# Optimization experiments

Measured on AMD Instinct MI355X. Metric: run time of the kernel, lower is better.

The kernel has to match this reference:

```python
import jax, jax.numpy as jnp
import numpy as np

B, M, T, F_IN, H = 16, 512, 64, 128, 128


def _gru_layer(x, wih, whh, bih, bhh):
    # x: [B, T, H_in]; torch nn.GRU gate math, single layer, h0 = 0
    Hh = whh.shape[1]

    def step(h_prev, x_t):
        gi = x_t @ wih.T + bih          # [B, 3H]
        gh = h_prev @ whh.T + bhh       # [B, 3H]
        i_r, i_z, i_n = jnp.split(gi, 3, axis=-1)
        h_r, h_z, h_n = jnp.split(gh, 3, axis=-1)
        r = jax.nn.sigmoid(i_r + h_r)
        z = jax.nn.sigmoid(i_z + h_z)
        n = jnp.tanh(i_n + r * h_n)
        h_new = (1.0 - z) * n + z * h_prev
        return h_new, h_new

    h0 = jnp.zeros((x.shape[0], Hh), x.dtype)
    _, ys = jax.lax.scan(step, h0, jnp.swapaxes(x, 0, 1))  # [T, B, H]
    return jnp.swapaxes(ys, 0, 1)                          # [B, T, H]


def setup_inputs() -> dict:
    key = jax.random.key(0)
    ks = jax.random.split(key, 12)
    s = 0.05

    def w(k, shape):
        return jax.random.normal(k, shape, jnp.float32) * s

    return {
        "X": jax.random.normal(ks[0], (B, M, T, F_IN), jnp.float32),
        "C": jax.random.normal(ks[1], (B, M, T), jnp.float32),
        "h_target": jax.random.normal(ks[2], (B, T, H), jnp.float32),
        "distance": jax.random.uniform(ks[3], (M,), jnp.float32),
        "lin_w": w(ks[4], (H, F_IN)), "lin_b": jnp.zeros((H,), jnp.float32),
        "mlp_w1": w(ks[5], (H, 2 * H)), "mlp_b1": jnp.zeros((H,), jnp.float32),
        "mlp_w2": w(ks[6], (1, H)), "mlp_b2": jnp.zeros((1,), jnp.float32),
        "lin2_w": w(ks[7], (1, 3)), "lin2_b": jnp.zeros((1,), jnp.float32),
        "gru_wih0": w(ks[8], (3 * H, H)), "gru_whh0": w(ks[9], (3 * H, H)),
        "gru_bih0": jnp.zeros((3 * H,), jnp.float32), "gru_bhh0": jnp.zeros((3 * H,), jnp.float32),
        "gru_wih1": w(ks[10], (3 * H, H)), "gru_whh1": w(ks[11], (3 * H, H)),
        "gru_bih1": jnp.zeros((3 * H,), jnp.float32), "gru_bhh1": jnp.zeros((3 * H,), jnp.float32),
    }


def reference(X, C, h_target, distance,
              lin_w, lin_b, mlp_w1, mlp_b1, mlp_w2, mlp_b2,
              lin2_w, lin2_b,
              gru_wih0, gru_whh0, gru_bih0, gru_bhh0,
              gru_wih1, gru_whh1, gru_bih1, gru_bhh1):
    # h: [B, M, T, H]
    h = jnp.einsum('bmtf,hf->bmth', X, lin_w) + lin_b
    # broadcast h_target over message dim M: [B, 1, T, H] -> [B, M, T, H]
    ht = jnp.broadcast_to(h_target[:, None, :, :], h.shape)
    cat = jnp.concatenate([ht, h], axis=-1)                    # [B, M, T, 2H]
    mlp_h = jax.nn.relu(jnp.einsum('bmtf,hf->bmth', cat, mlp_w1) + mlp_b1)
    w_msg = jnp.einsum('bmth,oh->bmto', mlp_h, mlp_w2) + mlp_b2  # [B, M, T, 1]
    # distance broadcast: [1, M, 1, 1] -> [B, M, T, 1]
    dist = jnp.broadcast_to(distance[None, :, None, None], w_msg.shape)
    coef = jnp.concatenate([C[..., None], dist, w_msg], axis=-1)  # [B, M, T, 3]
    learned_w = coef @ lin2_w.T + lin2_b                          # [B, M, T, 1]
    h_agg = jnp.sum(h * learned_w, axis=1)                        # [B, T, H]
    # 2-layer GRU (eval mode: no dropout)
    out0 = _gru_layer(h_agg, gru_wih0, gru_whh0, gru_bih0, gru_bhh0)
    out1 = _gru_layer(out0, gru_wih1, gru_whh1, gru_bih1, gru_bhh1)
    return out1
```

## Files before the change

### kernel.cpp

```cpp
#include <hip/hip_runtime.h>
#include <math.h>

#define NB 16
#define NM 512
#define NT 64
#define NF 128
#define NH 128
#define PADB 136

typedef short short8 __attribute__((ext_vector_type(8)));
typedef float floatx4 __attribute__((ext_vector_type(4)));

static __device__ __forceinline__ unsigned short f2b(float f) {
  union { float f; unsigned u; } v; v.f = f;
  unsigned r = v.u + 0x7fff + ((v.u >> 16) & 1);
  return (unsigned short)(r >> 16);
}
static __device__ __forceinline__ float b2f_us(unsigned short h) {
  union { unsigned u; float f; } v; v.u = ((unsigned)h) << 16; return v.f;
}

__global__ __launch_bounds__(128) void prep_kernel(
    const float* __restrict__ lin_w, const float* __restrict__ mlp_w1,
    const float* __restrict__ lin_b, const float* __restrict__ mlp_b1,
    unsigned short* __restrict__ WxBf, float* __restrict__ linT,
    float* __restrict__ ubase)
{
  const int tid = threadIdx.x;
  if (blockIdx.x < 128) {
    const int i = blockIdx.x;
    __shared__ float sw[128];
    __shared__ float rb[128];
    sw[tid] = mlp_w1[i * 256 + 128 + tid];
    __syncthreads();
    float s = 0.f;
#pragma unroll 16
    for (int k = 0; k < 128; k++) s += sw[k] * lin_w[k * 128 + tid];
    WxBf[i * 128 + tid] = f2b(s);
    rb[tid] = sw[tid] * lin_b[tid];
    __syncthreads();
    if (tid == 0) {
      float s2 = 0.f;
      for (int k = 0; k < 128; k++) s2 += rb[k];
      ubase[i] = mlp_b1[i] + s2;
    }
  } else {
    const int f = blockIdx.x - 128;
    linT[f * 128 + tid] = lin_w[tid * 128 + f];
  }
}

static __device__ __forceinline__ void tpose_tile(
    const float* __restrict__ in, float* __restrict__ outT,
    int R, int C, int S, int tileIdx)
{
  __shared__ float tile[32][33];
  const int tilesC = C >> 5;
  const int tr = tileIdx / tilesC, tc = tileIdx % tilesC;
  const int x = threadIdx.x & 31, y = threadIdx.x >> 5;
#pragma unroll
  for (int yy = y; yy < 32; yy += 8)
    tile[yy][x] = in[(size_t)(tr * 32 + yy) * S + tc * 32 + x];
  __syncthreads();
#pragma unroll
  for (int yy = y; yy < 32; yy += 8)
    outT[(size_t)(tc * 32 + yy) * R + tr * 32 + x] = tile[x][yy];
}

__global__ __launch_bounds__(256) void tpose_kernel(
    const float* __restrict__ wih0, const float* __restrict__ whh0,
    const float* __restrict__ wih1, const float* __restrict__ whh1,
    const float* __restrict__ mlp_w1,
    float* __restrict__ wih0T, float* __restrict__ whh0T,
    float* __restrict__ wih1T, float* __restrict__ whh1T,
    float* __restrict__ W1aT)
{
  const int b = blockIdx.x;
  if (b < 48)        tpose_tile(wih0,   wih0T, 384, 128, 128, b);
  else if (b < 96)   tpose_tile(whh0,   whh0T, 384, 128, 128, b - 48);
  else if (b < 144)  tpose_tile(wih1,   wih1T, 384, 128, 128, b - 96);
  else if (b < 192)  tpose_tile(whh1,   whh1T, 384, 128, 128, b - 144);
  else               tpose_tile(mlp_w1, W1aT,  128, 128, 256, b - 192);
}

__global__ __launch_bounds__(128) void u_kernel(
    const float* __restrict__ h_target, const float* __restrict__ W1aT,
    const float* __restrict__ ubase, float* __restrict__ u_out)
{
  const int bt = blockIdx.x, i = threadIdx.x;
  __shared__ float sht[128];
  sht[i] = h_target[bt * 128 + i];
  __syncthreads();
  float u = ubase[i];
#pragma unroll 16
  for (int k = 0; k < 128; k++) u += W1aT[k * 128 + i] * sht[k];
  u_out[bt * 128 + i] = u;
}

__global__ __launch_bounds__(256, 2) void pass1_kernel(
    const float* __restrict__ X, const float* __restrict__ C,
    const float* __restrict__ dist,
    const unsigned short* __restrict__ WxBf, const float* __restrict__ u_g,
    const float* __restrict__ mlp_w2, const float* __restrict__ mlp_b2,
    const float* __restrict__ lin2_w, const float* __restrict__ lin2_b,
    float* __restrict__ part, float* __restrict__ partls)
{
  const int blk = blockIdx.x;
  const int g = blk & 7, bt = blk >> 3;
  const int b = bt >> 6, t = bt & 63;
  const int tid = threadIdx.x;

  __shared__ unsigned short xb[64 * PADB];
  __shared__ unsigned short wxb[128 * PADB];
  __shared__ float u_sh[128], w2_sh[128], lw_sh[64];
  __shared__ float red[2][128];
  __shared__ float red_ls;

  const float* Xbase = X + (((size_t)(b * NM + g * 64)) * NT + t) * NF;
#pragma unroll
  for (int p = 0; p < 8; p++) {
    int idx = p * 256 + tid;
    int row = idx >> 5, c4 = idx & 31;
    float4 xv = *(const float4*)(Xbase + (size_t)row * NT * NF + c4 * 4);
    ushort4 h;
    h.x = f2b(xv.x); h.y = f2b(xv.y); h.z = f2b(xv.z); h.w = f2b(xv.w);
    *(ushort4*)&xb[row * PADB + c4 * 4] = h;
  }
  const unsigned* wsrc = (const unsigned*)WxBf;
  unsigned* wdst = (unsigned*)wxb;
#pragma unroll
  for (int p = 0; p < 32; p++) {
    int idx = p * 256 + tid;
    int row = idx >> 6, cu = idx & 63;
    wdst[row * (PADB / 2) + cu] = wsrc[idx];
  }
  if (tid < 128) { u_sh[tid] = u_g[bt * 128 + tid]; w2_sh[tid] = mlp_w2[tid]; }
  __syncthreads();

  const int w = tid >> 6, lane = tid & 63;
  const int col = lane & 15, quad = lane >> 4;
  short8 afr[4];
#pragma unroll
  for (int kc = 0; kc < 4; kc++)
    afr[kc] = *(const short8*)&xb[(w * 16 + col) * PADB + kc * 32 + quad * 8];
  floatx4 acc[8];
#pragma unroll
  for (int it = 0; it < 8; it++) acc[it] = {0.f, 0.f, 0.f, 0.f};
#pragma unroll
  for (int it = 0; it < 8; it++) {
#pragma unroll
    for (int kc = 0; kc < 4; kc++) {
      short8 bfr = *(const short8*)&wxb[(it * 16 + col) * PADB + kc * 32 + quad * 8];
      acc[it] = __builtin_amdgcn_mfma_f32_16x16x32_bf16(afr[kc], bfr, acc[it], 0, 0, 0);
    }
  }

  float w2l[8], ul[8];
#pragma unroll
  for (int it = 0; it < 8; it++) { w2l[it] = w2_sh[it * 16 + col]; ul[it] = u_sh[it * 16 + col]; }
  float vsum[4];
#pragma unroll
  for (int r = 0; r < 4; r++) {
    float v = 0.f;
#pragma unroll
    for (int it = 0; it < 8; it++) {
      float s = acc[it][r] + ul[it];
      v += w2l[it] * fmaxf(s, 0.f);
    }
    v += __shfl_xor(v, 1, 64);
    v += __shfl_xor(v, 2, 64);
    v += __shfl_xor(v, 4, 64);
    v += __shfl_xor(v, 8, 64);
    vsum[r] = v;
  }
  if (col == 0) {
    const float c0 = lin2_w[0], c1 = lin2_w[1], c2 = lin2_w[2];
    const float lb2 = lin2_b[0], mb2 = mlp_b2[0];
#pragma unroll
    for (int r = 0; r < 4; r++) {
      int ml = w * 16 + quad * 4 + r;
      int m = g * 64 + ml;
      float wmsg = vsum[r] + mb2;
      lw_sh[ml] = C[((size_t)b * NM + m) * NT + t] * c0 + dist[m] * c1 + wmsg * c2 + lb2;
    }
  }
  __syncthreads();

  const int f = tid & 127, half = tid >> 7;
  float xa = 0.f;
#pragma unroll 8
  for (int mm = half * 32; mm < half * 32 + 32; mm++)
    xa += lw_sh[mm] * b2f_us(xb[mm * PADB + f]);
  red[half][f] = xa;
  if (tid < 64) {
    float v = lw_sh[tid];
    v += __shfl_xor(v, 1, 64);
    v += __shfl_xor(v, 2, 64);
    v += __shfl_xor(v, 4, 64);
    v += __shfl_xor(v, 8, 64);
    v += __shfl_xor(v, 16, 64);
    v += __shfl_xor(v, 32, 64);
    if (tid == 0) red_ls = v;
  }
  __syncthreads();
  if (tid < 128) part[(size_t)blk * 128 + tid] = red[0][tid] + red[1][tid];
  if (tid == 128) partls[blk] = red_ls;
}

__global__ __launch_bounds__(384) void reduce_kernel(
    const float* __restrict__ part, const float* __restrict__ partls,
    const float* __restrict__ linT, const float* __restrict__ lin_b,
    const float* __restrict__ wih0T, const float* __restrict__ bih0,
    float* __restrict__ gi0)
{
  const int bt = blockIdx.x, j = threadIdx.x;
  __shared__ float sxa[128], shh[128];
  __shared__ float sls;
  if (j < 128) {
    float s = 0.f;
#pragma unroll
    for (int g2 = 0; g2 < 8; g2++) s += part[((size_t)bt * 8 + g2) * 128 + j];
    sxa[j] = s;
  }
  if (j == 128) {
    float s = 0.f;
#pragma unroll
    for (int g2 = 0; g2 < 8; g2++) s += partls[bt * 8 + g2];
    sls = s;
  }
  __syncthreads();
  if (j < 128) {
    float hv = sls * lin_b[j];
#pragma unroll 8
    for (int f2 = 0; f2 < 128; f2++) hv += linT[f2 * 128 + j] * sxa[f2];
    shh[j] = hv;
  }
  __syncthreads();
  float gacc = bih0[j];
#pragma unroll 16
  for (int k = 0; k < 128; k++) gacc += wih0T[k * 384 + j] * shh[k];
  gi0[(size_t)bt * 384 + j] = gacc;
}

__global__ __launch_bounds__(384, 2) void gi_kernel(
    const float* __restrict__ xin, const float* __restrict__ wihT,
    const float* __restrict__ bih, float* __restrict__ gi)
{
  __shared__ __align__(16) float xr[128];
  const int bt = blockIdx.x, j = threadIdx.x;
  if (j < 128) xr[j] = xin[bt * 128 + j];
  __syncthreads();
  float a0 = 0.f, a1 = 0.f, a2 = 0.f, a3 = 0.f;
#pragma unroll 8
  for (int k = 0; k < 128; k += 4) {
    a0 += wihT[(k    ) * 384 + j] * xr[k];
    a1 += wihT[(k + 1) * 384 + j] * xr[k + 1];
    a2 += wihT[(k + 2) * 384 + j] * xr[k + 2];
    a3 += wihT[(k + 3) * 384 + j] * xr[k + 3];
  }
  gi[(size_t)bt * 384 + j] = (a0 + a1) + (a2 + a3) + bih[j];
}

__global__ __launch_bounds__(384, 1) void gru_layer_kernel(
    const float* __restrict__ gi, const float* __restrict__ whhT,
    const float* __restrict__ bhh, float* __restrict__ out)
{
  const int b = blockIdx.x, j = threadIdx.x;
  __shared__ float sgi[64 * 384];
  __shared__ float hs[128], ghs[384];

  const float4* gsrc = (const float4*)(gi + (size_t)b * 64 * 384);
  float4* gdst = (float4*)sgi;
#pragma unroll
  for (int p = 0; p < 16; p++) gdst[p * 384 + j] = gsrc[p * 384 + j];

  float wreg[128];
#pragma unroll
  for (int k = 0; k < 128; k++) wreg[k] = whhT[k * 384 + j];
  const float bh = bhh[j];
  if (j < 128) hs[j] = 0.f;
  __syncthreads();

  for (int t = 0; t < NT; t++) {
    float a0 = 0.f, a1 = 0.f, a2 = 0.f, a3 = 0.f;
    const float4* h4 = (const float4*)hs;
#pragma unroll
    for (int k = 0; k < 32; k++) {
      float4 hv = h4[k];
      a0 += wreg[4 * k]     * hv.x;
      a1 += wreg[4 * k + 1] * hv.y;
      a2 += wreg[4 * k + 2] * hv.z;
      a3 += wreg[4 * k + 3] * hv.w;
    }
    ghs[j] = (a0 + a1) + (a2 + a3) + bh;
    __syncthreads();
    if (j < 128) {
      const float* gt = &sgi[t * 384];
      const float hprev = hs[j];
      const float r = 1.f / (1.f + __expf(-(gt[j] + ghs[j])));
      const float z = 1.f / (1.f + __expf(-(gt[128 + j] + ghs[128 + j])));
      float nx = gt[256 + j] + r * ghs[256 + j];
      nx = fmaxf(fminf(nx, 15.f), -15.f);
      const float e2 = __expf(2.f * nx);
      const float n = (e2 - 1.f) / (e2 + 1.f);
      const float hnew = (1.f - z) * n + z * hprev;
      hs[j] = hnew;
      out[((size_t)b * NT + t) * 128 + j] = hnew;
    }
    __syncthreads();
  }
}

extern "C" void kernel_launch(void* const* d_in, const int* in_sizes, int n_in,
                              void* d_out, int out_size, void* d_ws, size_t ws_size,
                              hipStream_t stream)
{
  const float* X        = (const float*)d_in[0];
  const float* C        = (const float*)d_in[1];
  const float* h_target = (const float*)d_in[2];
  const float* distance = (const float*)d_in[3];
  const float* lin_w    = (const float*)d_in[4];
  const float* lin_b    = (const float*)d_in[5];
  const float* mlp_w1   = (const float*)d_in[6];
  const float* mlp_b1   = (const float*)d_in[7];
  const float* mlp_w2   = (const float*)d_in[8];
  const float* mlp_b2   = (const float*)d_in[9];
  const float* lin2_w   = (const float*)d_in[10];
  const float* lin2_b   = (const float*)d_in[11];
  const float* wih0     = (const float*)d_in[12];
  const float* whh0     = (const float*)d_in[13];
  const float* bih0     = (const float*)d_in[14];
  const float* bhh0     = (const float*)d_in[15];
  const float* wih1     = (const float*)d_in[16];
  const float* whh1     = (const float*)d_in[17];
  const float* bih1     = (const float*)d_in[18];
  const float* bhh1     = (const float*)d_in[19];
  float* out = (float*)d_out;

  float* ws = (float*)d_ws;
  unsigned short* WxBf = (unsigned short*)ws;
  float* linT   = ws + 8192;
  float* u_buf  = ws + 24576;
  float* part   = ws + 155648;
  float* partls = ws + 1204224;
  float* gi     = ws + 1212416;
  float* out0   = ws + 1605632;
  float* W1aT   = ws + 1736704;
  float* wih0T  = ws + 1753088;
  float* whh0T  = ws + 1802240;
  float* wih1T  = ws + 1851392;
  float* whh1T  = ws + 1900544;
  float* ubase  = ws + 1949696;

  prep_kernel<<<256, 128, 0, stream>>>(lin_w, mlp_w1, lin_b, mlp_b1, WxBf, linT, ubase);
  tpose_kernel<<<208, 256, 0, stream>>>(wih0, whh0, wih1, whh1, mlp_w1,
      wih0T, whh0T, wih1T, whh1T, W1aT);
  u_kernel<<<NB * NT, 128, 0, stream>>>(h_target, W1aT, ubase, u_buf);
  pass1_kernel<<<NB * NT * 8, 256, 0, stream>>>(X, C, distance, WxBf, u_buf,
      mlp_w2, mlp_b2, lin2_w, lin2_b, part, partls);
  reduce_kernel<<<NB * NT, 384, 0, stream>>>(part, partls, linT, lin_b, wih0T, bih0, gi);
  gru_layer_kernel<<<NB, 384, 0, stream>>>(gi, whh0T, bhh0, out0);
  gi_kernel<<<NB * NT, 384, 0, stream>>>(out0, wih1T, bih1, gi);
  gru_layer_kernel<<<NB, 384, 0, stream>>>(gi, whh1T, bhh1, out);
}
```

Before: 605.8 us.

## Pre-swizzle weight fragments in global memory and keep X tile in fp32 LDS

The fused weight matrix is written by the prep kernel directly in MFMA B-fragment order, so pass1 reads B fragments straight from global/L2 instead of staging the whole weight matrix into LDS each block. X is kept in fp32 in LDS and converted to bf16 when the A fragments are built, so the aggregation step now uses fp32 X instead of the bf16-rounded values. With less LDS per block, the occupancy hint is raised from 2 to 4 blocks. The GRU gate math switches from fast __expf with manual tanh to expf/tanhf, which is more accurate but likely slower in the serial recurrence.

```diff
diff --git a/kernel.cpp b/kernel.cpp
--- a/kernel.cpp
+++ b/kernel.cpp
@@ -6,7 +6,7 @@
 #define NT 64
 #define NF 128
 #define NH 128
-#define PADB 136
+#define PAD4 132
 
 typedef short short8 __attribute__((ext_vector_type(8)));
 typedef float floatx4 __attribute__((ext_vector_type(4)));
@@ -16,14 +16,11 @@
   unsigned r = v.u + 0x7fff + ((v.u >> 16) & 1);
   return (unsigned short)(r >> 16);
 }
-static __device__ __forceinline__ float b2f_us(unsigned short h) {
-  union { unsigned u; float f; } v; v.u = ((unsigned)h) << 16; return v.f;
-}
 
 __global__ __launch_bounds__(128) void prep_kernel(
     const float* __restrict__ lin_w, const float* __restrict__ mlp_w1,
     const float* __restrict__ lin_b, const float* __restrict__ mlp_b1,
-    unsigned short* __restrict__ WxBf, float* __restrict__ linT,
+    unsigned short* __restrict__ WxFrag, float* __restrict__ linT,
     float* __restrict__ ubase)
 {
   const int tid = threadIdx.x;
@@ -36,7 +33,12 @@
     float s = 0.f;
 #pragma unroll 16
     for (int k = 0; k < 128; k++) s += sw[k] * lin_w[k * 128 + tid];
-    WxBf[i * 128 + tid] = f2b(s);
+    {
+      const int it = i >> 4, col = i & 15;
+      const int f = tid;
+      const int kc = f >> 5, quad = (f >> 3) & 3, jj = f & 7;
+      WxFrag[((it * 4 + kc) * 64 + quad * 16 + col) * 8 + jj] = f2b(s);
+    }
     rb[tid] = sw[tid] * lin_b[tid];
     __syncthreads();
     if (tid == 0) {
@@ -97,10 +99,10 @@
   u_out[bt * 128 + i] = u;
 }
 
-__global__ __launch_bounds__(256, 2) void pass1_kernel(
+__global__ __launch_bounds__(256, 4) void pass1_kernel(
     const float* __restrict__ X, const float* __restrict__ C,
     const float* __restrict__ dist,
-    const unsigned short* __restrict__ WxBf, const float* __restrict__ u_g,
+    const unsigned short* __restrict__ WxFrag, const float* __restrict__ u_g,
     const float* __restrict__ mlp_w2, const float* __restrict__ mlp_b2,
     const float* __restrict__ lin2_w, const float* __restrict__ lin2_b,
     float* __restrict__ part, float* __restrict__ partls)
@@ -110,8 +112,7 @@
   const int b = bt >> 6, t = bt & 63;
   const int tid = threadIdx.x;
 
-  __shared__ unsigned short xb[64 * PADB];
-  __shared__ unsigned short wxb[128 * PADB];
+  __shared__ float xs[64 * PAD4];
   __shared__ float u_sh[128], w2_sh[128], lw_sh[64];
   __shared__ float red[2][128];
   __shared__ float red_ls;
@@ -122,17 +123,7 @@
     int idx = p * 256 + tid;
     int row = idx >> 5, c4 = idx & 31;
     float4 xv = *(const float4*)(Xbase + (size_t)row * NT * NF + c4 * 4);
-    ushort4 h;
-    h.x = f2b(xv.x); h.y = f2b(xv.y); h.z = f2b(xv.z); h.w = f2b(xv.w);
-    *(ushort4*)&xb[row * PADB + c4 * 4] = h;
-  }
-  const unsigned* wsrc = (const unsigned*)WxBf;
-  unsigned* wdst = (unsigned*)wxb;
-#pragma unroll
-  for (int p = 0; p < 32; p++) {
-    int idx = p * 256 + tid;
-    int row = idx >> 6, cu = idx & 63;
-    wdst[row * (PADB / 2) + cu] = wsrc[idx];
+    *(float4*)&xs[row * PAD4 + c4 * 4] = xv;
   }
   if (tid < 128) { u_sh[tid] = u_g[bt * 128 + tid]; w2_sh[tid] = mlp_w2[tid]; }
   __syncthreads();
@@ -141,8 +132,13 @@
   const int col = lane & 15, quad = lane >> 4;
   short8 afr[4];
 #pragma unroll
-  for (int kc = 0; kc < 4; kc++)
-    afr[kc] = *(const short8*)&xb[(w * 16 + col) * PADB + kc * 32 + quad * 8];
+  for (int kc = 0; kc < 4; kc++) {
+    const float* src = &xs[(w * 16 + col) * PAD4 + kc * 32 + quad * 8];
+    short8 a;
+#pragma unroll
+    for (int jv = 0; jv < 8; jv++) a[jv] = (short)f2b(src[jv]);
+    afr[kc] = a;
+  }
   floatx4 acc[8];
 #pragma unroll
   for (int it = 0; it < 8; it++) acc[it] = {0.f, 0.f, 0.f, 0.f};
@@ -150,7 +146,7 @@
   for (int it = 0; it < 8; it++) {
 #pragma unroll
     for (int kc = 0; kc < 4; kc++) {
-      short8 bfr = *(const short8*)&wxb[(it * 16 + col) * PADB + kc * 32 + quad * 8];
+      short8 bfr = *(const short8*)&WxFrag[((it * 4 + kc) * 64 + lane) * 8];
       acc[it] = __builtin_amdgcn_mfma_f32_16x16x32_bf16(afr[kc], bfr, acc[it], 0, 0, 0);
     }
   }
@@ -190,7 +186,7 @@
   float xa = 0.f;
 #pragma unroll 8
   for (int mm = half * 32; mm < half * 32 + 32; mm++)
-    xa += lw_sh[mm] * b2f_us(xb[mm * PADB + f]);
+    xa += lw_sh[mm] * xs[mm * PAD4 + f];
   red[half][f] = xa;
   if (tid < 64) {
     float v = lw_sh[tid];
@@ -297,12 +293,9 @@
     if (j < 128) {
       const float* gt = &sgi[t * 384];
       const float hprev = hs[j];
-      const float r = 1.f / (1.f + __expf(-(gt[j] + ghs[j])));
-      const float z = 1.f / (1.f + __expf(-(gt[128 + j] + ghs[128 + j])));
-      float nx = gt[256 + j] + r * ghs[256 + j];
-      nx = fmaxf(fminf(nx, 15.f), -15.f);
-      const float e2 = __expf(2.f * nx);
-      const float n = (e2 - 1.f) / (e2 + 1.f);
+      const float r = 1.f / (1.f + expf(-(gt[j] + ghs[j])));
+      const float z = 1.f / (1.f + expf(-(gt[128 + j] + ghs[128 + j])));
+      const float n = tanhf(gt[256 + j] + r * ghs[256 + j]);
       const float hnew = (1.f - z) * n + z * hprev;
       hs[j] = hnew;
       out[((size_t)b * NT + t) * 128 + j] = hnew;
@@ -338,7 +331,7 @@
   float* out = (float*)d_out;
 
   float* ws = (float*)d_ws;
-  unsigned short* WxBf = (unsigned short*)ws;
+  unsigned short* WxFrag = (unsigned short*)ws;
   float* linT   = ws + 8192;
   float* u_buf  = ws + 24576;
   float* part   = ws + 155648;
@@ -352,11 +345,11 @@
   float* whh1T  = ws + 1900544;
   float* ubase  = ws + 1949696;
 
-  prep_kernel<<<256, 128, 0, stream>>>(lin_w, mlp_w1, lin_b, mlp_b1, WxBf, linT, ubase);
+  prep_kernel<<<256, 128, 0, stream>>>(lin_w, mlp_w1, lin_b, mlp_b1, WxFrag, linT, ubase);
   tpose_kernel<<<208, 256, 0, stream>>>(wih0, whh0, wih1, whh1, mlp_w1,
       wih0T, whh0T, wih1T, whh1T, W1aT);
   u_kernel<<<NB * NT, 128, 0, stream>>>(h_target, W1aT, ubase, u_buf);
-  pass1_kernel<<<NB * NT * 8, 256, 0, stream>>>(X, C, distance, WxBf, u_buf,
+  pass1_kernel<<<NB * NT * 8, 256, 0, stream>>>(X, C, distance, WxFrag, u_buf,
       mlp_w2, mlp_b2, lin2_w, lin2_b, part, partls);
   reduce_kernel<<<NB * NT, 384, 0, stream>>>(part, partls, linT, lin_b, wih0T, bih0, gi);
   gru_layer_kernel<<<NB, 384, 0, stream>>>(gi, whh0T, bhh0, out0);
```

New measurement: 619.3 us. 2.2% more time.
